# Kernel tuning notes

Hardware: AMD Instinct MI355X
Metric: run time of the kernel (lower is better)

The kernel has to match this reference:

```python
import jax, jax.numpy as jnp
import numpy as np

N = 4096  # flattened_input_shape


def setup_inputs() -> dict:
    key = jax.random.key(0)
    ks = jax.random.split(key, 5)
    eps = 0.1
    center = jax.random.normal(ks[0], (1, N), dtype=jnp.float32)
    lb0 = center - eps  # initial interval lower bounds [1, N]
    ub0 = center + eps  # initial interval upper bounds [1, N]
    W1 = jax.random.normal(ks[1], (N, N), dtype=jnp.float32) / np.float32(np.sqrt(N))
    b1 = jax.random.normal(ks[2], (1, N), dtype=jnp.float32)
    W2 = jax.random.normal(ks[3], (N, N), dtype=jnp.float32) / np.float32(np.sqrt(N))
    b2 = jax.random.normal(ks[4], (1, N), dtype=jnp.float32)
    raw_alpha = jnp.ones((N,), dtype=jnp.float32)  # nn.Parameter init
    return {"raw_alpha": raw_alpha, "lb0": lb0, "ub0": ub0,
            "W1": W1, "b1": b1, "W2": W2, "b2": b2}


def _pos(x):
    return jnp.where(x > 0, x, jnp.zeros_like(x))


def _neg(x):
    return jnp.where(x < 0, x, jnp.zeros_like(x))


def _forward(raw_alpha, lb0, ub0, W1, b1, W2, b2):
    # ---- previous.backsubstitution(): compose affine2 over affine1 ----
    clslope, clintercept = W2, b2
    cuslope, cuintercept = W2, b2
    clp, cln = _pos(clslope), _neg(clslope)
    cup, cun = _pos(cuslope), _neg(cuslope)
    clintercept = b1 @ clp.T + b1 @ cln.T + clintercept  # [1, N]
    cuintercept = b1 @ cup.T + b1 @ cun.T + cuintercept  # [1, N]
    clslope = clp @ W1 + cln @ W1  # [N, N]
    cuslope = cup @ W1 + cun @ W1  # [N, N]
    # ---- certifier against initial interval bounds ----
    lbounds = lb0 @ _pos(clslope).T + ub0 @ _neg(clslope).T + clintercept  # [1, N]
    ubounds = ub0 @ _pos(cuslope).T + lb0 @ _neg(cuslope).T + cuintercept  # [1, N]
    # ---- DeepPolyReLU transformer ----
    alpha = jax.nn.sigmoid(raw_alpha)  # [N]
    lb = lbounds.reshape(-1)
    ub = ubounds.reshape(-1)
    denom = ub - lb
    # ub/(ub-lb) with NaN (0/0) replaced by 0, grad-safe
    relu_slope = jnp.where(denom == 0, 0.0, ub / jnp.where(denom == 0, 1.0, denom))  # [N]
    relu_intercept = (1.0 - relu_slope)[None, :] * ubounds  # [1, N]
    below = ub <= 0
    above = lb >= 0
    crossing = ~(below | above)
    base = jnp.where(above, 1.0, 0.0)  # [N]
    uslope = jnp.where(crossing, relu_slope, base)
    uintercept = jnp.where(crossing[None, :], relu_intercept, jnp.zeros((1, N), dtype=ubounds.dtype))
    lslope_v1 = jnp.where(crossing, 0.0, base)
    lslope_v2 = jnp.where(crossing, 1.0, base)
    lslope = alpha * lslope_v1 + (1.0 - alpha) * lslope_v2  # [N]
    lintercept = jnp.zeros((1, N), dtype=lbounds.dtype)
    return jnp.diag(lslope), lintercept, jnp.diag(uslope), uintercept


def reference(raw_alpha, lb0, ub0, W1, b1, W2, b2):
    return _forward(raw_alpha, lb0, ub0, W1, b1, W2, b2)
```

## Files before the change

### kernel.cpp

```cpp
#include <hip/hip_runtime.h>
#include <stdint.h>

#define N 4096

#define TILE_BYTES 524288
#define KT_BYTES   16384

#define QSCALE 256.0f
#define INV_QQ (1.0f / 65536.0f)

typedef int v8i __attribute__((ext_vector_type(8)));
typedef float f32x16 __attribute__((ext_vector_type(16)));
typedef unsigned int u32x4 __attribute__((ext_vector_type(4)));

union V8 { v8i v; u32x4 h[2]; };

__device__ __forceinline__ void gload16(const unsigned char* g, unsigned char* l) {
  __builtin_amdgcn_global_load_lds(
      (const __attribute__((address_space(1))) unsigned int*)g,
      (__attribute__((address_space(3))) unsigned int*)l, 16, 0, 0);
}

__device__ __forceinline__ int pack4_fp8(float a, float b, float c, float d) {
  int r = __builtin_amdgcn_cvt_pk_fp8_f32(a, b, 0, false);
  r = __builtin_amdgcn_cvt_pk_fp8_f32(c, d, r, true);
  return r;
}

__global__ __launch_bounds__(256) void prep_w1(const float* __restrict__ W1,
                                               const float* __restrict__ lb0,
                                               const float* __restrict__ ub0,
                                               unsigned char* __restrict__ W1T,
                                               float* __restrict__ tvec) {
  __shared__ float tile[64 * 65];
  __shared__ float tdot[64];
  const int t = threadIdx.x;
  const int j0 = blockIdx.x * 64, k0 = blockIdx.y * 64;
#pragma unroll
  for (int s = 0; s < 4; ++s) {
    int ck = s * 256 + t;
    int row = ck >> 4;
    int col = (ck & 15) * 4;
    float4 v = *(const float4*)(W1 + (size_t)(k0 + row) * N + j0 + col);
    float4 l = *(const float4*)(lb0 + j0 + col);
    float4 u = *(const float4*)(ub0 + j0 + col);
    float part = v.x * 0.5f * (l.x + u.x) + v.y * 0.5f * (l.y + u.y)
               + v.z * 0.5f * (l.z + u.z) + v.w * 0.5f * (l.w + u.w);
    part += __shfl_xor(part, 1, 64);
    part += __shfl_xor(part, 2, 64);
    part += __shfl_xor(part, 4, 64);
    part += __shfl_xor(part, 8, 64);
    if ((t & 15) == 0) tdot[row] = part;
    float* d = &tile[row * 65 + col];
    d[0] = v.x; d[1] = v.y; d[2] = v.z; d[3] = v.w;
  }
  __syncthreads();
  if (t < 64) atomicAdd(&tvec[k0 + t], tdot[t]);
  int jl = t >> 2, ch = (t & 3) * 16;
  float f[16];
#pragma unroll
  for (int m = 0; m < 16; ++m) f[m] = tile[(ch + m) * 65 + jl] * QSCALE;
  uint4 o;
  o.x = (unsigned)pack4_fp8(f[0], f[1], f[2], f[3]);
  o.y = (unsigned)pack4_fp8(f[4], f[5], f[6], f[7]);
  o.z = (unsigned)pack4_fp8(f[8], f[9], f[10], f[11]);
  o.w = (unsigned)pack4_fp8(f[12], f[13], f[14], f[15]);
  int j = j0 + jl;
  int kb = k0 + ch;
  *(uint4*)(W1T + (size_t)(j >> 7) * TILE_BYTES + (size_t)(kb >> 7) * KT_BYTES
            + (size_t)((kb >> 4) & 7) * 2048 + (j & 127) * 16) = o;
}

__global__ __launch_bounds__(256) void convert_w2(const float* __restrict__ W2,
                                                  const float* __restrict__ b1,
                                                  const float* __restrict__ tvec,
                                                  unsigned char* __restrict__ W2q,
                                                  float* __restrict__ cvec,
                                                  float* __restrict__ Sc) {
  __shared__ int lpack[128][33];
  const int t = threadIdx.x;
  const int i0 = blockIdx.y * 128;
  const int k0 = blockIdx.x * 128;
  const int kl = (t & 31) * 4;
  const int rsub = t >> 5;
  float4 bv = *(const float4*)(b1 + k0 + kl);
  float4 tv = *(const float4*)(tvec + k0 + kl);
#pragma unroll
  for (int s = 0; s < 16; ++s) {
    int row = s * 8 + rsub;
    float4 w = *(const float4*)(W2 + (size_t)(i0 + row) * N + k0 + kl);
    float db = w.x * bv.x + w.y * bv.y + w.z * bv.z + w.w * bv.w;
    float dt = w.x * tv.x + w.y * tv.y + w.z * tv.z + w.w * tv.w;
    db += __shfl_xor(db, 1, 64);  dt += __shfl_xor(dt, 1, 64);
    db += __shfl_xor(db, 2, 64);  dt += __shfl_xor(dt, 2, 64);
    db += __shfl_xor(db, 4, 64);  dt += __shfl_xor(dt, 4, 64);
    db += __shfl_xor(db, 8, 64);  dt += __shfl_xor(dt, 8, 64);
    db += __shfl_xor(db, 16, 64); dt += __shfl_xor(dt, 16, 64);
    if ((t & 31) == 0) {
      atomicAdd(&cvec[i0 + row], db);
      atomicAdd(&Sc[i0 + row], dt);
    }
    lpack[row][t & 31] = pack4_fp8(w.x * QSCALE, w.y * QSCALE,
                                   w.z * QSCALE, w.w * QSCALE);
  }
  __syncthreads();
  unsigned char* panel = W2q + (size_t)blockIdx.y * TILE_BYTES
                       + (size_t)blockIdx.x * KT_BYTES;
#pragma unroll
  for (int q = 0; q < 4; ++q) {
    int cid = q * 256 + t;
    int r = cid & 127, c = cid >> 7;
    uint4 o;
    o.x = (unsigned)lpack[r][4 * c + 0];
    o.y = (unsigned)lpack[r][4 * c + 1];
    o.z = (unsigned)lpack[r][4 * c + 2];
    o.w = (unsigned)lpack[r][4 * c + 3];
    *(uint4*)(panel + (size_t)c * 2048 + r * 16) = o;
  }
}

#define DSR(dst, addr, OFF) \
  asm volatile("ds_read_b128 %0, %1 offset:" OFF : "=v"(dst) : "v"(addr))

__global__ __launch_bounds__(512, 2) void gemm_absrow(const unsigned char* __restrict__ A,
                                                      const unsigned char* __restrict__ B,
                                                      const float* __restrict__ lb0,
                                                      const float* __restrict__ ub0,
                                                      float* __restrict__ R_acc) {
  __shared__ __align__(16) unsigned char sm[4 * 32768];
  const int t = threadIdx.x;
  const int lane = t & 63, w = t >> 6;
  const int wr = w >> 2, wc = w & 3;
  const int l31 = lane & 31, half = lane >> 5;

  const int bid = blockIdx.y * 16 + blockIdx.x;
  const int swz = (bid & 7) * 32 + (bid >> 3);
  const int bm = swz >> 4, bn = swz & 15;
  const int i0 = bm * 256, j0 = bn * 256;

  const unsigned char* gA0 = A + (size_t)(2 * bm) * TILE_BYTES + t * 16;
  const unsigned char* gA1 = gA0 + TILE_BYTES;
  const unsigned char* gB0 = B + (size_t)(2 * bn) * TILE_BYTES + t * 16;
  const unsigned char* gB1 = gB0 + TILE_BYTES;

  f32x16 acc[4][2] = {};
  const int sc1 = 0x7F7F7F7F;

  const unsigned lds0 =
      (unsigned)(size_t)(__attribute__((address_space(3))) unsigned char*)sm;
  const unsigned aoff = lds0 + wr * 8192 + half * 4096 + l31 * 16;
  const int jb0 = wc * 64 + l31, jb1 = jb0 + 32;
  const unsigned boff0 = lds0 + 16384 + (jb0 >> 7) * 8192 + half * 4096 + (jb0 & 127) * 16;
  const unsigned boff1 = lds0 + 16384 + (jb1 >> 7) * 8192 + half * 4096 + (jb1 & 127) * 16;

  auto stage = [&](int g) {
    unsigned char* d = sm + (size_t)(g & 3) * 32768 + t * 16;
    const size_t off = (size_t)(g >> 1) * KT_BYTES + (size_t)(g & 1) * 8192;
    gload16(gA0 + off, d);
    gload16(gA1 + off, d + 8192);
    gload16(gB0 + off, d + 16384);
    gload16(gB1 + off, d + 24576);
  };

  V8 af[4], bf[2];

#define PHASE_LOAD(g)                                                     \
  {                                                                       \
    unsigned sb = (unsigned)((g) & 3) * 32768u;                           \
    unsigned sa = aoff + sb, s0 = boff0 + sb, s1 = boff1 + sb;            \
    DSR(af[0].h[0], sa, "0");    DSR(af[0].h[1], sa, "2048");             \
    DSR(bf[0].h[0], s0, "0");    DSR(bf[0].h[1], s0, "2048");             \
    DSR(bf[1].h[0], s1, "0");    DSR(bf[1].h[1], s1, "2048");             \
    DSR(af[1].h[0], sa, "512");  DSR(af[1].h[1], sa, "2560");             \
    DSR(af[2].h[0], sa, "1024"); DSR(af[2].h[1], sa, "3072");             \
    DSR(af[3].h[0], sa, "1536"); DSR(af[3].h[1], sa, "3584");             \
  }

#define MFMA2(tm)                                                         \
  acc[tm][0] = __builtin_amdgcn_mfma_scale_f32_32x32x64_f8f6f4(           \
      af[tm].v, bf[0].v, acc[tm][0], 0, 0, 0, sc1, 0, sc1);               \
  acc[tm][1] = __builtin_amdgcn_mfma_scale_f32_32x32x64_f8f6f4(           \
      af[tm].v, bf[1].v, acc[tm][1], 0, 0, 0, sc1, 0, sc1);

#define PHASE_MFMA()                                                      \
  __builtin_amdgcn_s_setprio(1);                                          \
  asm volatile("s_waitcnt lgkmcnt(6)" ::: "memory");                      \
  __builtin_amdgcn_sched_barrier(0);                                      \
  MFMA2(0)                                                                \
  asm volatile("s_waitcnt lgkmcnt(4)" ::: "memory");                      \
  __builtin_amdgcn_sched_barrier(0);                                      \
  MFMA2(1)                                                                \
  asm volatile("s_waitcnt lgkmcnt(2)" ::: "memory");                      \
  __builtin_amdgcn_sched_barrier(0);                                      \
  MFMA2(2)                                                                \
  asm volatile("s_waitcnt lgkmcnt(0)" ::: "memory");                      \
  __builtin_amdgcn_sched_barrier(0);                                      \
  MFMA2(3)                                                                \
  __builtin_amdgcn_s_setprio(0);

  stage(0); stage(1); stage(2);

#pragma unroll 1
  for (int g = 0; g < 61; ++g) {
    asm volatile("s_waitcnt vmcnt(8)" ::: "memory");
    __builtin_amdgcn_s_barrier();
    PHASE_LOAD(g);
    stage(g + 3);
    PHASE_MFMA();
  }
  asm volatile("s_waitcnt vmcnt(8)" ::: "memory");
  __builtin_amdgcn_s_barrier();
  PHASE_LOAD(61);
  PHASE_MFMA();
  asm volatile("s_waitcnt vmcnt(4)" ::: "memory");
  __builtin_amdgcn_s_barrier();
  PHASE_LOAD(62);
  PHASE_MFMA();
  asm volatile("s_waitcnt vmcnt(0)" ::: "memory");
  __builtin_amdgcn_s_barrier();
  PHASE_LOAD(63);
  PHASE_MFMA();

  float epsv[2];
#pragma unroll
  for (int tn = 0; tn < 2; ++tn) {
    int j = j0 + wc * 64 + tn * 32 + l31;
    epsv[tn] = 0.5f * (ub0[j] - lb0[j]);
  }
#pragma unroll
  for (int tm = 0; tm < 4; ++tm) {
#pragma unroll
    for (int r = 0; r < 16; ++r) {
      float s = fabsf(acc[tm][0][r]) * epsv[0] + fabsf(acc[tm][1][r]) * epsv[1];
#pragma unroll
      for (int off = 1; off < 32; off <<= 1)
        s += __shfl_xor(s, off, 64);
      if (l31 == 0) {
        int i = i0 + wr * 128 + tm * 32 + (r & 3) + 8 * (r >> 2) + 4 * half;
        atomicAdd(&R_acc[i], s);
      }
    }
  }
}

struct ReluVals { float lslope, uslope, uinter; };

__device__ __forceinline__ ReluVals relu_vals(int i,
                                              const float* __restrict__ cvec,
                                              const float* __restrict__ Sc,
                                              const float* __restrict__ b2,
                                              const float* __restrict__ R_acc,
                                              const float* __restrict__ raw_alpha) {
  float mid = Sc[i] + cvec[i] + b2[i];
  float rr = R_acc[i] * INV_QQ;
  float lb = mid - rr;
  float ub = mid + rr;
  float alpha = 1.f / (1.f + expf(-raw_alpha[i]));
  float denom = ub - lb;
  float slope = (denom == 0.f) ? 0.f : ub / denom;
  bool below = ub <= 0.f, above = lb >= 0.f;
  bool crossing = !(below || above);
  float base = above ? 1.f : 0.f;
  ReluVals v;
  v.uslope = crossing ? slope : base;
  v.uinter = crossing ? (1.f - slope) * ub : 0.f;
  float l1 = crossing ? 0.f : base;
  float l2 = crossing ? 1.f : base;
  v.lslope = alpha * l1 + (1.f - alpha) * l2;
  return v;
}

__global__ __launch_bounds__(256) void patch_diag(float* __restrict__ out,
                                                  const float* __restrict__ cvec,
                                                  const float* __restrict__ Sc,
                                                  const float* __restrict__ b2,
                                                  const float* __restrict__ R_acc,
                                                  const float* __restrict__ raw_alpha) {
  const size_t NN = (size_t)N * N;
  int i = blockIdx.x * 256 + threadIdx.x;
  ReluVals v = relu_vals(i, cvec, Sc, b2, R_acc, raw_alpha);
  out[(size_t)i * (N + 1)] = v.lslope;
  out[NN + N + (size_t)i * (N + 1)] = v.uslope;
  out[2 * NN + N + i] = v.uinter;
}

extern "C" void kernel_launch(void* const* d_in, const int* in_sizes, int n_in,
                              void* d_out, int out_size, void* d_ws, size_t ws_size,
                              hipStream_t stream) {
  const float* raw_alpha = (const float*)d_in[0];
  const float* lb0 = (const float*)d_in[1];
  const float* ub0 = (const float*)d_in[2];
  const float* W1 = (const float*)d_in[3];
  const float* b1 = (const float*)d_in[4];
  const float* W2 = (const float*)d_in[5];
  const float* b2 = (const float*)d_in[6];

  float* tvec = (float*)d_ws;
  float* cvec = tvec + N;
  float* Sc = cvec + N;
  float* R_acc = Sc + N;

  unsigned char* W2q = (unsigned char*)d_out;
  unsigned char* W1Tq = W2q + (size_t)N * N;

  (void)hipMemsetAsync(d_ws, 0, 4 * N * sizeof(float), stream);
  prep_w1<<<dim3(N / 64, N / 64), 256, 0, stream>>>(W1, lb0, ub0, W1Tq, tvec);
  convert_w2<<<dim3(N / 128, N / 128), 256, 0, stream>>>(W2, b1, tvec, W2q, cvec, Sc);
  gemm_absrow<<<dim3(16, 16), 512, 0, stream>>>(W2q, W1Tq, lb0, ub0, R_acc);
  (void)hipMemsetAsync(d_out, 0, (size_t)out_size * sizeof(float), stream);
  patch_diag<<<N / 256, 256, 0, stream>>>((float*)d_out, cvec, Sc, b2, R_acc, raw_alpha);
}
```

Measured before the change: 338.0 us.

## Replace hand-scheduled GEMM pipeline with simpler double-buffered compute lambda

The FP8 GEMM main loop drops the inline-asm ds_read macros and the staggered lgkmcnt waits that interleaved LDS reads with MFMAs. In their place is a per-half-tile compute lambda using plain LDS loads and a prefetch of the next k-tile, so loads run about two half-stages ahead instead of three. This simplifies the code and hands scheduling back to the compiler, at the risk of less overlap between LDS reads, global loads and matrix ops. Separately, the W1 transpose kernel remaps threads so consecutive threads handle consecutive columns, which should make the packed FP8 stores coalesced.

```diff
diff --git a/kernel.cpp b/kernel.cpp
--- a/kernel.cpp
+++ b/kernel.cpp
@@ -56,7 +56,7 @@
   }
   __syncthreads();
   if (t < 64) atomicAdd(&tvec[k0 + t], tdot[t]);
-  int jl = t >> 2, ch = (t & 3) * 16;
+  int jl = t & 63, ch = (t >> 6) * 16;
   float f[16];
 #pragma unroll
   for (int m = 0; m < 16; ++m) f[m] = tile[(ch + m) * 65 + jl] * QSCALE;
@@ -119,9 +119,7 @@
   }
 }
 
-#define DSR(dst, addr, OFF) \
-  asm volatile("ds_read_b128 %0, %1 offset:" OFF : "=v"(dst) : "v"(addr))
-
+#define NT 32
 __global__ __launch_bounds__(512, 2) void gemm_absrow(const unsigned char* __restrict__ A,
                                                       const unsigned char* __restrict__ B,
                                                       const float* __restrict__ lb0,
@@ -146,80 +144,67 @@
   f32x16 acc[4][2] = {};
   const int sc1 = 0x7F7F7F7F;
 
-  const unsigned lds0 =
-      (unsigned)(size_t)(__attribute__((address_space(3))) unsigned char*)sm;
-  const unsigned aoff = lds0 + wr * 8192 + half * 4096 + l31 * 16;
-  const int jb0 = wc * 64 + l31, jb1 = jb0 + 32;
-  const unsigned boff0 = lds0 + 16384 + (jb0 >> 7) * 8192 + half * 4096 + (jb0 & 127) * 16;
-  const unsigned boff1 = lds0 + 16384 + (jb1 >> 7) * 8192 + half * 4096 + (jb1 & 127) * 16;
-
-  auto stage = [&](int g) {
-    unsigned char* d = sm + (size_t)(g & 3) * 32768 + t * 16;
-    const size_t off = (size_t)(g >> 1) * KT_BYTES + (size_t)(g & 1) * 8192;
+  auto stage = [&](int kt, int h) {
+    const int g = ((kt & 1) << 1) | h;
+    unsigned char* d = sm + g * 32768 + t * 16;
+    const size_t off = (size_t)kt * KT_BYTES + (size_t)h * 8192;
     gload16(gA0 + off, d);
     gload16(gA1 + off, d + 8192);
     gload16(gB0 + off, d + 16384);
     gload16(gB1 + off, d + 24576);
   };
 
-  V8 af[4], bf[2];
-
-#define PHASE_LOAD(g)                                                     \
-  {                                                                       \
-    unsigned sb = (unsigned)((g) & 3) * 32768u;                           \
-    unsigned sa = aoff + sb, s0 = boff0 + sb, s1 = boff1 + sb;            \
-    DSR(af[0].h[0], sa, "0");    DSR(af[0].h[1], sa, "2048");             \
-    DSR(bf[0].h[0], s0, "0");    DSR(bf[0].h[1], s0, "2048");             \
-    DSR(bf[1].h[0], s1, "0");    DSR(bf[1].h[1], s1, "2048");             \
-    DSR(af[1].h[0], sa, "512");  DSR(af[1].h[1], sa, "2560");             \
-    DSR(af[2].h[0], sa, "1024"); DSR(af[2].h[1], sa, "3072");             \
-    DSR(af[3].h[0], sa, "1536"); DSR(af[3].h[1], sa, "3584");             \
-  }
-
-#define MFMA2(tm)                                                         \
-  acc[tm][0] = __builtin_amdgcn_mfma_scale_f32_32x32x64_f8f6f4(           \
-      af[tm].v, bf[0].v, acc[tm][0], 0, 0, 0, sc1, 0, sc1);               \
-  acc[tm][1] = __builtin_amdgcn_mfma_scale_f32_32x32x64_f8f6f4(           \
-      af[tm].v, bf[1].v, acc[tm][1], 0, 0, 0, sc1, 0, sc1);
-
-#define PHASE_MFMA()                                                      \
-  __builtin_amdgcn_s_setprio(1);                                          \
-  asm volatile("s_waitcnt lgkmcnt(6)" ::: "memory");                      \
-  __builtin_amdgcn_sched_barrier(0);                                      \
-  MFMA2(0)                                                                \
-  asm volatile("s_waitcnt lgkmcnt(4)" ::: "memory");                      \
-  __builtin_amdgcn_sched_barrier(0);                                      \
-  MFMA2(1)                                                                \
-  asm volatile("s_waitcnt lgkmcnt(2)" ::: "memory");                      \
-  __builtin_amdgcn_sched_barrier(0);                                      \
-  MFMA2(2)                                                                \
-  asm volatile("s_waitcnt lgkmcnt(0)" ::: "memory");                      \
-  __builtin_amdgcn_sched_barrier(0);                                      \
-  MFMA2(3)                                                                \
-  __builtin_amdgcn_s_setprio(0);
-
-  stage(0); stage(1); stage(2);
-
-#pragma unroll 1
-  for (int g = 0; g < 61; ++g) {
-    asm volatile("s_waitcnt vmcnt(8)" ::: "memory");
-    __builtin_amdgcn_s_barrier();
-    PHASE_LOAD(g);
-    stage(g + 3);
-    PHASE_MFMA();
-  }
-  asm volatile("s_waitcnt vmcnt(8)" ::: "memory");
-  __builtin_amdgcn_s_barrier();
-  PHASE_LOAD(61);
-  PHASE_MFMA();
+  auto compute = [&](int kt, int h) {
+    const unsigned char* base = sm + (((kt & 1) << 1) | h) * 32768;
+    V8 af[4], bf[2];
+    const unsigned char* pa = base + wr * 8192 + (half * 2) * 2048 + l31 * 16;
+#pragma unroll
+    for (int tm = 0; tm < 4; ++tm) {
+      const unsigned char* p = pa + tm * 512;
+      af[tm].h[0] = *(const u32x4*)p;
+      af[tm].h[1] = *(const u32x4*)(p + 2048);
+    }
+#pragma unroll
+    for (int tn = 0; tn < 2; ++tn) {
+      const int j = wc * 64 + tn * 32 + l31;
+      const unsigned char* p = base + 16384 + (j >> 7) * 8192
+                             + (half * 2) * 2048 + (j & 127) * 16;
+      bf[tn].h[0] = *(const u32x4*)p;
+      bf[tn].h[1] = *(const u32x4*)(p + 2048);
+    }
+    __builtin_amdgcn_s_setprio(1);
+#pragma unroll
+    for (int tm = 0; tm < 4; ++tm)
+#pragma unroll
+      for (int tn = 0; tn < 2; ++tn)
+        acc[tm][tn] = __builtin_amdgcn_mfma_scale_f32_32x32x64_f8f6f4(
+            af[tm].v, bf[tn].v, acc[tm][tn],
+            0 , 0 ,
+            0, sc1, 0, sc1);
+    __builtin_amdgcn_s_setprio(0);
+  };
+
+  stage(0, 0);
+  stage(0, 1);
+
+  for (int kt = 0; kt < NT - 1; ++kt) {
+#pragma unroll
+    for (int h = 0; h < 2; ++h) {
+      stage(kt + 1, h);
+      asm volatile("s_waitcnt vmcnt(8)" ::: "memory");
+      __builtin_amdgcn_s_barrier();
+      asm volatile("" ::: "memory");
+      compute(kt, h);
+    }
+  }
   asm volatile("s_waitcnt vmcnt(4)" ::: "memory");
   __builtin_amdgcn_s_barrier();
-  PHASE_LOAD(62);
-  PHASE_MFMA();
+  asm volatile("" ::: "memory");
+  compute(NT - 1, 0);
   asm volatile("s_waitcnt vmcnt(0)" ::: "memory");
   __builtin_amdgcn_s_barrier();
-  PHASE_LOAD(63);
-  PHASE_MFMA();
+  asm volatile("" ::: "memory");
+  compute(NT - 1, 1);
 
   float epsv[2];
 #pragma unroll
```

New measurement: 339.6 us. About the same (+0.5%).
